# Optimization experiments

Hardware: AMD Instinct MI355X
Metric: run time of the kernel (lower is better)

The kernel has to match this reference:

```python
import jax, jax.numpy as jnp
import numpy as np

B, T, N = 512, 1024, 48


def setup_inputs() -> dict:
    key = jax.random.key(0)
    k1, k2, k3, k4 = jax.random.split(key, 4)
    potentials = jax.random.normal(k1, (B, T, N), dtype=jnp.float32)
    y_true = jax.random.randint(k2, (B, T), 0, N, dtype=jnp.int32)
    lengths = jax.random.randint(k3, (B,), 1, T + 1, dtype=jnp.int32)
    transitions = jax.random.normal(k4, (N, N), dtype=jnp.float32)
    return {"potentials": potentials, "y_true": y_true,
            "lengths": lengths, "transitions": transitions}


def _crf_log_likelihood(potentials, tags, lengths, trans):
    # potentials: [B,T,N], tags: [B,T] int, lengths: [B] int, trans: [N,N]
    Bv, Tv, Nv = potentials.shape
    t_idx = jnp.arange(Tv)

    # ---- numerator: score of the given tag sequence ----
    unary = jnp.take_along_axis(potentials, tags[..., None], axis=2)[..., 0]  # [B,T]
    unary_mask = (t_idx[None, :] < lengths[:, None]).astype(potentials.dtype)
    unary_score = jnp.sum(unary * unary_mask, axis=1)  # [B]

    trans_scores = trans[tags[:, :-1], tags[:, 1:]]  # [B,T-1]
    pair_mask = (t_idx[None, 1:] < lengths[:, None]).astype(potentials.dtype)
    binary_score = jnp.sum(trans_scores * pair_mask, axis=1)  # [B]
    seq_score = unary_score + binary_score

    # ---- log partition: forward algorithm with length masking ----
    alpha0 = potentials[:, 0, :]  # [B,N]
    pots_rest = jnp.transpose(potentials[:, 1:, :], (1, 0, 2))  # [T-1,B,N]
    valid = (t_idx[1:, None] < lengths[None, :])  # [T-1,B]

    def step(alpha, inp):
        pot_t, v = inp  # [B,N], [B]
        # logsumexp over previous state: alpha[b,i] + trans[i,j]
        new_alpha = jax.nn.logsumexp(alpha[:, :, None] + trans[None, :, :], axis=1) + pot_t
        alpha = jnp.where(v[:, None], new_alpha, alpha)
        return alpha, None

    alpha_final, _ = jax.lax.scan(step, alpha0, (pots_rest, valid))
    log_norm = jax.nn.logsumexp(alpha_final, axis=-1)  # [B]

    return seq_score - log_norm


def reference(potentials, y_true, lengths, transitions):
    ll = _crf_log_likelihood(potentials, y_true.astype(jnp.int32),
                             lengths.astype(jnp.int32), transitions)
    return -ll  # per-sample NLL, shape [B]
```

## Files before the change

### kernel.cpp

```cpp
#include <hip/hip_runtime.h>
#include <cstdint>
#include <cstddef>

constexpr int Bb = 512;
constexpr int Tt = 1024;
constexpr int Nn = 48;
constexpr int SG = 16;
constexpr int NG = Bb / SG;
constexpr int Cc = 64;
constexpr int Lc = Tt / Cc;
constexpr int Wb = 32;
constexpr int TILE = 3328;

typedef short bf16x8 __attribute__((ext_vector_type(8)));
typedef float f32x4  __attribute__((ext_vector_type(4)));
typedef unsigned int u32x4 __attribute__((ext_vector_type(4)));

__device__ __forceinline__ unsigned int bf16_rne(float x) {
    const unsigned int u = __float_as_uint(x);
    return ((u + 0x7FFFu + ((u >> 16) & 1u)) >> 16);
}
__device__ __forceinline__ unsigned int pack2(float lo, float hi) {
    return bf16_rne(lo) | (bf16_rne(hi) << 16);
}
__device__ __forceinline__ float safe_log(float x) {
    return __logf(fmaxf(x, 1e-30f));
}
__device__ __forceinline__ void gll16(const float* g, const char* l) {
    __builtin_amdgcn_global_load_lds(
        (const __attribute__((address_space(1))) void*)g,
        (__attribute__((address_space(3))) void*)l, 16, 0, 0);
}

__launch_bounds__(64)
__global__ void crf_fused(const float* __restrict__ pot,
                          const int*   __restrict__ ytrue,
                          const int*   __restrict__ lengths,
                          const float* __restrict__ trans,
                          float*       __restrict__ out)
{
    __shared__ __align__(16) char smem_c[4 * TILE];
    float* trans_lds = (float*)smem_c;

    const int lane = threadIdx.x;
    const int ln   = lane & 15;
    const int q    = lane >> 4;
    const int gidx = blockIdx.x >> 6;
    const int c    = blockIdx.x & 63;
    const int s0   = gidx * SG;

    for (int i = lane; i < Nn * Nn; i += 64) trans_lds[i] = trans[i];
    __syncthreads();

    {
        const int    b    = blockIdx.x >> 2;
        const int    h    = blockIdx.x & 3;
        const int    lenb = lengths[b];
        const int*   yrow = ytrue + (size_t)b * Tt;
        const float* prow = pot + (size_t)b * Tt * Nn;
        float gold = 0.0f;
#pragma unroll
        for (int k = 0; k < Tt / 256; ++k) {
            const int   t    = h * (Tt / 4) + lane + 64 * k;
            const int   yt   = yrow[t];
            const int   ytm1 = yrow[(t > 0) ? (t - 1) : 0];
            const float u    = prow[(size_t)t * Nn + yt];
            const float tr   = trans_lds[ytm1 * Nn + yt];
            gold += (t < lenb) ? u : 0.0f;
            gold += (t >= 1 && t < lenb) ? tr : 0.0f;
        }
#pragma unroll
        for (int off = 32; off > 0; off >>= 1) gold += __shfl_xor(gold, off);
        if (lane == 0) atomicAdd(&out[b], -gold);
    }

    const int len_ln = lengths[s0 + ln];
    int lmax = len_ln;
#pragma unroll
    for (int off = 8; off > 0; off >>= 1) {
        const int o = __shfl_xor(lmax, off);
        lmax = (o > lmax) ? o : lmax;
    }

    const int start = (c == 0) ? 1 : c * Lc;
    if (c > 0 && start >= lmax) return;
    const int end = ((c + 1) * Lc < lmax) ? (c + 1) * Lc : lmax;

    bf16x8 Wf[3][2];
#pragma unroll
    for (int nt = 0; nt < 3; ++nt)
#pragma unroll
        for (int kc = 0; kc < 2; ++kc)
#pragma unroll
            for (int d = 0; d < 8; ++d) {
                int i;
                if (kc == 0) {
                    i = 16 * (d >> 2) + 4 * q + (d & 3);
                } else {
                    i = (q < 2) ? (32 + 8 * q + d) : -1;
                }
                const float v = (i >= 0) ? __expf(trans_lds[i * Nn + nt * 16 + ln]) : 0.0f;
                Wf[nt][kc][d] = (short)bf16_rne(v);
            }

    const int slA = ((2 * q) & 3) * 16 + ln;
    const int slB = slA + 16;
    const int slC = ln;

    const float* prow = pot + (size_t)(s0 + ln) * (Tt * Nn);
    const float* pp0 = prow + 0 * 16 + q * 4;
    const float* pp1 = prow + 1 * 16 + q * 4;
    const float* pp2 = prow + 2 * 16 + q * 4;

    int t0 = (c == 0) ? 1 : (start - Wb);
    if (t0 < 1) t0 = 1;

    f32x4 pin0 = *(const f32x4*)(pp0 + (size_t)(t0 - 1) * Nn);
    f32x4 pin1 = *(const f32x4*)(pp1 + (size_t)(t0 - 1) * Nn);
    f32x4 pin2 = *(const f32x4*)(pp2 + (size_t)(t0 - 1) * Nn);
    const float cb0 = __shfl(pin0[0], slC);

    float gacc = (c == 0) ? cb0 : 0.0f;
    f32x4 prev0, prev1, prev2;
#pragma unroll
    for (int r = 0; r < 4; ++r) {
        prev0[r] = __expf(pin0[r] - cb0);
        prev1[r] = __expf(pin1[r] - cb0);
        prev2[r] = __expf(pin2[r] - cb0);
    }

    unsigned int pk00 = pack2(prev0[0], prev0[1]);
    unsigned int pk01 = pack2(prev0[2], prev0[3]);
    unsigned int pk10 = pack2(prev1[0], prev1[1]);
    unsigned int pk11 = pack2(prev1[2], prev1[3]);
    unsigned int pk20 = pack2(prev2[0], prev2[1]);
    unsigned int pk21 = pack2(prev2[2], prev2[3]);
    bf16x8 Bf0 = __builtin_bit_cast(bf16x8, (u32x4){pk00, pk01, pk10, pk11});
    bf16x8 Bf1 = __builtin_bit_cast(bf16x8, (u32x4){
        (unsigned int)__shfl((int)pk20, slA), (unsigned int)__shfl((int)pk21, slA),
        (unsigned int)__shfl((int)pk20, slB), (unsigned int)__shfl((int)pk21, slB)});

    const float* srcp[4];
#pragma unroll
    for (int i = 0; i < 4; ++i) {
        int g = 64 * i + lane;
        int s = g / 13;  if (s > 15) s = 15;
        int cg = g % 13; if (cg > 11) cg = 11;
        srcp[i] = pot + (size_t)(s0 + s) * (Tt * Nn) + 4 * cg;
    }

    __syncthreads();

#define STAGE(tt, SLOT) do {                                                    \
        const size_t toff_ = (size_t)(((tt) < Tt) ? (tt) : (Tt - 1)) * Nn;      \
        char* lb_ = smem_c + (SLOT) * TILE;                                     \
        gll16(srcp[0] + toff_, lb_);                                            \
        gll16(srcp[1] + toff_, lb_ + 1024);                                     \
        gll16(srcp[2] + toff_, lb_ + 2048);                                     \
        if (lane < 16) gll16(srcp[3] + toff_, lb_ + 3072);                      \
    } while (0)

#define BOUNDARY(KK) do {                                                       \
        asm volatile("s_waitcnt vmcnt(0)" ::: "memory");                        \
        STAGE(t0 + (KK) + 2, ((KK) + 2) & 3);                                   \
        STAGE(t0 + (KK) + 3, ((KK) + 3) & 3);                                   \
    } while (0)

    const int lnq13 = ln * 13 + q;
    float rrp = 1.0f;

    STAGE(t0 + 0, 0);
    STAGE(t0 + 1, 1);

    const int ksteps = ((end - t0) + 3) & ~3;

#define CRF_STEP(KK, SLOT)                                                      \
    {                                                                           \
        const int t_ = t0 + (KK);                                               \
        const f32x4* tp_ = (const f32x4*)(smem_c + (SLOT) * TILE);              \
        const f32x4 PA_ = tp_[lnq13];                                           \
        const f32x4 PB_ = tp_[lnq13 + 4];                                       \
        const f32x4 PC_ = tp_[lnq13 + 8];                                       \
        f32x4 z_ = {0.0f, 0.0f, 0.0f, 0.0f};                                    \
        f32x4 D0_ = __builtin_amdgcn_mfma_f32_16x16x32_bf16(Wf[0][0], Bf0, z_, 0, 0, 0); \
        f32x4 D1_ = __builtin_amdgcn_mfma_f32_16x16x32_bf16(Wf[1][0], Bf0, z_, 0, 0, 0); \
        f32x4 D2_ = __builtin_amdgcn_mfma_f32_16x16x32_bf16(Wf[2][0], Bf0, z_, 0, 0, 0); \
        D0_ = __builtin_amdgcn_mfma_f32_16x16x32_bf16(Wf[0][1], Bf1, D0_, 0, 0, 0); \
        D1_ = __builtin_amdgcn_mfma_f32_16x16x32_bf16(Wf[1][1], Bf1, D1_, 0, 0, 0); \
        D2_ = __builtin_amdgcn_mfma_f32_16x16x32_bf16(Wf[2][1], Bf1, D2_, 0, 0, 0); \
        f32x4 a0_, a1_, a2_;                                                    \
        _Pragma("unroll")                                                       \
        for (int r = 0; r < 4; ++r) {                                           \
            a0_[r] = D0_[r] * (__expf(PA_[r]) * rrp);                           \
            a1_[r] = D1_[r] * (__expf(PB_[r]) * rrp);                           \
            a2_[r] = D2_[r] * (__expf(PC_[r]) * rrp);                           \
        }                                                                       \
        const float cb_ = __shfl(a0_[0], slC);                                  \
        const float rr_ = __builtin_amdgcn_rcpf(fmaxf(cb_, 1e-30f));            \
        const float lg_ = safe_log(cb_);                                        \
        gacc += ((t_ >= start) && (t_ < end) && (t_ + 1 < len_ln)) ? lg_ : 0.0f; \
        const bool act_ = (t_ < len_ln);                                        \
        _Pragma("unroll")                                                       \
        for (int r = 0; r < 4; ++r) {                                           \
            prev0[r] = act_ ? a0_[r] : prev0[r];                                \
            prev1[r] = act_ ? a1_[r] : prev1[r];                                \
            prev2[r] = act_ ? a2_[r] : prev2[r];                                \
        }                                                                       \
        pk00 = pack2(prev0[0], prev0[1]);                                       \
        pk01 = pack2(prev0[2], prev0[3]);                                       \
        pk10 = pack2(prev1[0], prev1[1]);                                       \
        pk11 = pack2(prev1[2], prev1[3]);                                       \
        pk20 = pack2(prev2[0], prev2[1]);                                       \
        pk21 = pack2(prev2[2], prev2[3]);                                       \
        Bf0 = __builtin_bit_cast(bf16x8, (u32x4){pk00, pk01, pk10, pk11});      \
        Bf1 = __builtin_bit_cast(bf16x8, (u32x4){                               \
            (unsigned int)__shfl((int)pk20, slA), (unsigned int)__shfl((int)pk21, slA), \
            (unsigned int)__shfl((int)pk20, slB), (unsigned int)__shfl((int)pk21, slB)}); \
        rrp = rr_;                                                              \
    }

    for (int k = 0; k < ksteps; k += 4) {
        BOUNDARY(k);
        CRF_STEP(k + 0, 0);
        CRF_STEP(k + 1, 1);
        BOUNDARY(k + 2);
        CRF_STEP(k + 2, 2);
        CRF_STEP(k + 3, 3);
    }
#undef CRF_STEP
#undef BOUNDARY
#undef STAGE

    asm volatile("s_waitcnt vmcnt(0)" ::: "memory");

    float rs = prev0[0] + prev0[1] + prev0[2] + prev0[3]
             + prev1[0] + prev1[1] + prev1[2] + prev1[3]
             + prev2[0] + prev2[1] + prev2[2] + prev2[3];
    rs += __shfl_xor(rs, 16);
    rs += __shfl_xor(rs, 32);

    const bool active_chunk = (c == 0) || (c * Lc < len_ln);
    const bool last = active_chunk && (len_ln <= (c + 1) * Lc);
    const float G = gacc + (last ? safe_log(rs) : 0.0f);
    if (lane < 16) atomicAdd(&out[s0 + ln], G);
}

extern "C" void kernel_launch(void* const* d_in, const int* in_sizes, int n_in,
                              void* d_out, int out_size, void* d_ws, size_t ws_size,
                              hipStream_t stream)
{
    const float* pot   = (const float*)d_in[0];
    const int*   ytrue = (const int*)  d_in[1];
    const int*   lens  = (const int*)  d_in[2];
    const float* trans = (const float*)d_in[3];
    float*       out   = (float*)d_out;

    hipMemsetAsync(out, 0, (size_t)out_size * sizeof(float), stream);
    crf_fused<<<dim3(NG * Cc), dim3(64), 0, stream>>>(pot, ytrue, lens, trans, out);
}
```

Measured before the change: 185.8 us.

## Deepen LDS prefetch ring to six slots and drop cross-lane shuffles in MFMA operand

Grows the LDS staging ring from four to six time-step slots, prefetches four steps ahead and waits with a partial vmcnt instead of draining all loads, so global-to-LDS copies overlap more of the serial recurrence. The second K-chunk weight fragment is re-laid out so each lane feeds its own packed values, removing four __shfl per step from the critical path. LDS reads now go through inline ds_read_b128 with explicit lgkmcnt waits and sched barriers. Block-to-group mapping is reordered and launch bounds request two waves per SIMD. Hand-counted vmcnt values and inline asm carry correctness risk if the instruction count differs from what is assumed.

Result: no change. 187.1 us (+0.7%).

```diff
diff --git a/kernel.cpp b/kernel.cpp
--- a/kernel.cpp
+++ b/kernel.cpp
@@ -11,6 +11,7 @@
 constexpr int Lc = Tt / Cc;
 constexpr int Wb = 32;
 constexpr int TILE = 3328;
+constexpr int NSLOT = 6;
 
 typedef short bf16x8 __attribute__((ext_vector_type(8)));
 typedef float f32x4  __attribute__((ext_vector_type(4)));
@@ -31,30 +32,32 @@
         (const __attribute__((address_space(1))) void*)g,
         (__attribute__((address_space(3))) void*)l, 16, 0, 0);
 }
-
-__launch_bounds__(64)
+#define DSR(dst, ad) asm volatile("ds_read_b128 %0, %1" : "=&v"(dst) : "v"(ad))
+
+__launch_bounds__(64, 2)
 __global__ void crf_fused(const float* __restrict__ pot,
                           const int*   __restrict__ ytrue,
                           const int*   __restrict__ lengths,
                           const float* __restrict__ trans,
                           float*       __restrict__ out)
 {
-    __shared__ __align__(16) char smem_c[4 * TILE];
+    __shared__ __align__(16) char smem_c[NSLOT * TILE];
     float* trans_lds = (float*)smem_c;
 
     const int lane = threadIdx.x;
     const int ln   = lane & 15;
     const int q    = lane >> 4;
-    const int gidx = blockIdx.x >> 6;
-    const int c    = blockIdx.x & 63;
+    const int w    = blockIdx.x;
+    const int gidx = (w & 7) * 4 + ((w >> 3) & 3);
+    const int c    = w >> 5;
     const int s0   = gidx * SG;
 
     for (int i = lane; i < Nn * Nn; i += 64) trans_lds[i] = trans[i];
     __syncthreads();
 
     {
-        const int    b    = blockIdx.x >> 2;
-        const int    h    = blockIdx.x & 3;
+        const int    b    = w >> 2;
+        const int    h    = w & 3;
         const int    lenb = lengths[b];
         const int*   yrow = ytrue + (size_t)b * Tt;
         const float* prow = pot + (size_t)b * Tt * Nn;
@@ -97,14 +100,12 @@
                 if (kc == 0) {
                     i = 16 * (d >> 2) + 4 * q + (d & 3);
                 } else {
-                    i = (q < 2) ? (32 + 8 * q + d) : -1;
+                    i = (d < 4) ? (32 + 4 * q + d) : -1;
                 }
                 const float v = (i >= 0) ? __expf(trans_lds[i * Nn + nt * 16 + ln]) : 0.0f;
                 Wf[nt][kc][d] = (short)bf16_rne(v);
             }
 
-    const int slA = ((2 * q) & 3) * 16 + ln;
-    const int slB = slA + 16;
     const int slC = ln;
 
     const float* prow = pot + (size_t)(s0 + ln) * (Tt * Nn);
@@ -136,9 +137,7 @@
     unsigned int pk20 = pack2(prev2[0], prev2[1]);
     unsigned int pk21 = pack2(prev2[2], prev2[3]);
     bf16x8 Bf0 = __builtin_bit_cast(bf16x8, (u32x4){pk00, pk01, pk10, pk11});
-    bf16x8 Bf1 = __builtin_bit_cast(bf16x8, (u32x4){
-        (unsigned int)__shfl((int)pk20, slA), (unsigned int)__shfl((int)pk21, slA),
-        (unsigned int)__shfl((int)pk20, slB), (unsigned int)__shfl((int)pk21, slB)});
+    bf16x8 Bf1 = __builtin_bit_cast(bf16x8, (u32x4){pk20, pk21, 0u, 0u});
 
     const float* srcp[4];
 #pragma unroll
@@ -148,6 +147,10 @@
         int cg = g % 13; if (cg > 11) cg = 11;
         srcp[i] = pot + (size_t)(s0 + s) * (Tt * Nn) + 4 * cg;
     }
+
+    typedef __attribute__((address_space(3))) char as3char;
+    const unsigned lbase  = (unsigned)(uintptr_t)(as3char*)smem_c;
+    const unsigned adbase = lbase + (unsigned)((ln * 13 + q) * 16);
 
     __syncthreads();
 
@@ -161,26 +164,30 @@
     } while (0)
 
 #define BOUNDARY(KK) do {                                                       \
-        asm volatile("s_waitcnt vmcnt(0)" ::: "memory");                        \
-        STAGE(t0 + (KK) + 2, ((KK) + 2) & 3);                                   \
-        STAGE(t0 + (KK) + 3, ((KK) + 3) & 3);                                   \
+        asm volatile("s_waitcnt vmcnt(8)");                                     \
+        __builtin_amdgcn_sched_barrier(0);                                      \
+        STAGE(t0 + (KK) + 4, ((KK) + 4) % NSLOT);                               \
+        STAGE(t0 + (KK) + 5, ((KK) + 5) % NSLOT);                               \
     } while (0)
 
-    const int lnq13 = ln * 13 + q;
     float rrp = 1.0f;
 
+    asm volatile("s_waitcnt vmcnt(0)");
     STAGE(t0 + 0, 0);
     STAGE(t0 + 1, 1);
-
-    const int ksteps = ((end - t0) + 3) & ~3;
+    STAGE(t0 + 2, 2);
+    STAGE(t0 + 3, 3);
+
+    const int ksteps = ((end - t0) + 5) / 6 * 6;
 
 #define CRF_STEP(KK, SLOT)                                                      \
     {                                                                           \
         const int t_ = t0 + (KK);                                               \
-        const f32x4* tp_ = (const f32x4*)(smem_c + (SLOT) * TILE);              \
-        const f32x4 PA_ = tp_[lnq13];                                           \
-        const f32x4 PB_ = tp_[lnq13 + 4];                                       \
-        const f32x4 PC_ = tp_[lnq13 + 8];                                       \
+        f32x4 PA_, PB_, PC_;                                                    \
+        const unsigned ad_ = adbase + (SLOT) * TILE;                            \
+        DSR(PA_, ad_);                                                          \
+        DSR(PB_, ad_ + 64u);                                                    \
+        DSR(PC_, ad_ + 128u);                                                   \
         f32x4 z_ = {0.0f, 0.0f, 0.0f, 0.0f};                                    \
         f32x4 D0_ = __builtin_amdgcn_mfma_f32_16x16x32_bf16(Wf[0][0], Bf0, z_, 0, 0, 0); \
         f32x4 D1_ = __builtin_amdgcn_mfma_f32_16x16x32_bf16(Wf[1][0], Bf0, z_, 0, 0, 0); \
@@ -188,6 +195,8 @@
         D0_ = __builtin_amdgcn_mfma_f32_16x16x32_bf16(Wf[0][1], Bf1, D0_, 0, 0, 0); \
         D1_ = __builtin_amdgcn_mfma_f32_16x16x32_bf16(Wf[1][1], Bf1, D1_, 0, 0, 0); \
         D2_ = __builtin_amdgcn_mfma_f32_16x16x32_bf16(Wf[2][1], Bf1, D2_, 0, 0, 0); \
+        asm volatile("s_waitcnt lgkmcnt(0)");                                   \
+        __builtin_amdgcn_sched_barrier(0);                                      \
         f32x4 a0_, a1_, a2_;                                                    \
         _Pragma("unroll")                                                       \
         for (int r = 0; r < 4; ++r) {                                           \
@@ -213,25 +222,20 @@
         pk20 = pack2(prev2[0], prev2[1]);                                       \
         pk21 = pack2(prev2[2], prev2[3]);                                       \
         Bf0 = __builtin_bit_cast(bf16x8, (u32x4){pk00, pk01, pk10, pk11});      \
-        Bf1 = __builtin_bit_cast(bf16x8, (u32x4){                               \
-            (unsigned int)__shfl((int)pk20, slA), (unsigned int)__shfl((int)pk21, slA), \
-            (unsigned int)__shfl((int)pk20, slB), (unsigned int)__shfl((int)pk21, slB)}); \
+        Bf1 = __builtin_bit_cast(bf16x8, (u32x4){pk20, pk21, 0u, 0u});          \
         rrp = rr_;                                                              \
     }
 
-    for (int k = 0; k < ksteps; k += 4) {
-        BOUNDARY(k);
-        CRF_STEP(k + 0, 0);
-        CRF_STEP(k + 1, 1);
-        BOUNDARY(k + 2);
-        CRF_STEP(k + 2, 2);
-        CRF_STEP(k + 3, 3);
+    for (int k = 0; k < ksteps; k += 6) {
+        BOUNDARY(k);     CRF_STEP(k + 0, 0); CRF_STEP(k + 1, 1);
+        BOUNDARY(k + 2); CRF_STEP(k + 2, 2); CRF_STEP(k + 3, 3);
+        BOUNDARY(k + 4); CRF_STEP(k + 4, 4); CRF_STEP(k + 5, 5);
     }
 #undef CRF_STEP
 #undef BOUNDARY
 #undef STAGE
 
-    asm volatile("s_waitcnt vmcnt(0)" ::: "memory");
+    asm volatile("s_waitcnt vmcnt(0)");
 
     float rs = prev0[0] + prev0[1] + prev0[2] + prev0[3]
              + prev1[0] + prev1[1] + prev1[2] + prev1[3]
```
